# Kernel optimization log

Measured on AMD Instinct MI355X. Metric: run time of the kernel, lower is better.

## Reference

```python
import jax, jax.numpy as jnp
import numpy as np

B, H, W = 32, 64, 1024
D, L, HEADS, E, TOPK, HID, V = 256, 6, 8, 8, 2, 1024, 8000


def _conv(x, w, b, s):
    y = jax.lax.conv_general_dilated(x, w, (s, s), [(1, 1), (1, 1)],
                                     dimension_numbers=('NCHW', 'OIHW', 'NCHW'))
    return y + b[None, :, None, None]


def _gelu(v):
    return jax.nn.gelu(v, approximate=False)


def _ln(x, g, b):
    m = x.mean(-1, keepdims=True)
    v = jnp.mean((x - m) ** 2, -1, keepdims=True)
    return (x - m) * jax.lax.rsqrt(v + 1e-5) * g + b


def _pos(t, c):
    pos = jnp.arange(t, dtype=jnp.float32)[:, None]
    div = jnp.exp(jnp.arange(0, c, 2, dtype=jnp.float32) * (-np.log(10000.0) / c))
    pe = jnp.zeros((t, c), jnp.float32)
    pe = pe.at[:, 0::2].set(jnp.sin(pos * div)).at[:, 1::2].set(jnp.cos(pos * div))
    return pe[None]


def _mha(y, w, b, ow, ob):
    Bq, T, Dm = y.shape
    hd = Dm // HEADS
    qkv = y @ w.T + b
    q, k, v = jnp.split(qkv, 3, axis=-1)
    sh = lambda z: z.reshape(Bq, T, HEADS, hd).transpose(0, 2, 1, 3)
    q, k, v = sh(q), sh(k), sh(v)
    att = jax.nn.softmax(jnp.einsum('bhqd,bhkd->bhqk', q, k) / np.sqrt(hd).astype(np.float32), axis=-1)
    o = jnp.einsum('bhqk,bhkd->bhqd', att, v).transpose(0, 2, 1, 3).reshape(Bq, T, Dm)
    return o @ ow.T + ob


def _moe(y, rw, rb, w1, b1, w2, b2):
    logits = y @ rw.T + rb                      # [B,T,E]
    tlog, tidx = jax.lax.top_k(logits, TOPK)
    gates = jax.nn.softmax(tlog, axis=-1)        # [B,T,K]
    # combine weights per expert: sum_k gate_k * 1[idx_k == e]
    comb = jnp.sum(gates[..., None] * jax.nn.one_hot(tidx, E, dtype=y.dtype), axis=-2)  # [B,T,E]
    h = _gelu(jnp.einsum('btd,ehd->beth', y, w1) + b1[None, :, None, :])
    eo = jnp.einsum('beth,edh->betd', h, w2) + b2[None, :, None, :]
    out = jnp.einsum('bte,betd->btd', comb, eo)
    imp = jax.nn.softmax(logits, axis=-1).mean(axis=(0, 1))
    aux = jnp.mean((imp - 1.0 / E) ** 2)
    return out, aux


def _forward(x, cw1, cb1, cw2, cb2, cw3, cb3, cw4, cb4,
             ln1_g, ln1_b, qkv_w, qkv_b, out_w, out_b,
             ln2_g, ln2_b, router_w, router_b, e_w1, e_b1, e_w2, e_b2,
             normf_g, normf_b, head_w, head_b):
    f = _gelu(_conv(x, cw1, cb1, 2))
    f = _gelu(_conv(f, cw2, cb2, 2))
    f = _gelu(_conv(f, cw3, cb3, 2))
    f = _gelu(_conv(f, cw4, cb4, 1))          # [B,D,H/8,W/8]
    tok = f.mean(axis=2).transpose(0, 2, 1)    # [B,T,D], T=W/8
    h = tok + _pos(tok.shape[1], tok.shape[2])
    aux_total = jnp.asarray(0.0, h.dtype)
    for l in range(L):
        y = _mha(_ln(h, ln1_g[l], ln1_b[l]), qkv_w[l], qkv_b[l], out_w[l], out_b[l])
        h = h + y
        y, aux = _moe(_ln(h, ln2_g[l], ln2_b[l]), router_w[l], router_b[l],
                      e_w1[l], e_b1[l], e_w2[l], e_b2[l])
        h = h + y
        aux_total = aux_total + aux
    h = _ln(h, normf_g, normf_b)
    logits = h @ head_w.T + head_b
    return logits, aux_total / L


def setup_inputs() -> dict:
    key = jax.random.key(0)
    ks = iter(jax.random.split(key, 40))
    nrm = lambda shape: jax.random.normal(next(ks), shape, jnp.float32) * 0.02
    d = {}
    d['x'] = jax.random.normal(next(ks), (B, 1, H, W), jnp.float32)
    d['cw1'] = nrm((D // 4, 1, 3, 3));      d['cb1'] = jnp.zeros((D // 4,), jnp.float32)
    d['cw2'] = nrm((D // 2, D // 4, 3, 3)); d['cb2'] = jnp.zeros((D // 2,), jnp.float32)
    d['cw3'] = nrm((D, D // 2, 3, 3));      d['cb3'] = jnp.zeros((D,), jnp.float32)
    d['cw4'] = nrm((D, D, 3, 3));           d['cb4'] = jnp.zeros((D,), jnp.float32)
    d['ln1_g'] = jnp.ones((L, D), jnp.float32); d['ln1_b'] = jnp.zeros((L, D), jnp.float32)
    d['qkv_w'] = nrm((L, 3 * D, D));        d['qkv_b'] = jnp.zeros((L, 3 * D), jnp.float32)
    d['out_w'] = nrm((L, D, D));            d['out_b'] = jnp.zeros((L, D), jnp.float32)
    d['ln2_g'] = jnp.ones((L, D), jnp.float32); d['ln2_b'] = jnp.zeros((L, D), jnp.float32)
    d['router_w'] = nrm((L, E, D));         d['router_b'] = jnp.zeros((L, E), jnp.float32)
    d['e_w1'] = nrm((L, E, HID, D));        d['e_b1'] = jnp.zeros((L, E, HID), jnp.float32)
    d['e_w2'] = nrm((L, E, D, HID));        d['e_b2'] = jnp.zeros((L, E, D), jnp.float32)
    d['normf_g'] = jnp.ones((D,), jnp.float32); d['normf_b'] = jnp.zeros((D,), jnp.float32)
    d['head_w'] = nrm((V, D));              d['head_b'] = jnp.zeros((V,), jnp.float32)
    return d


def reference(x, cw1, cb1, cw2, cb2, cw3, cb3, cw4, cb4,
              ln1_g, ln1_b, qkv_w, qkv_b, out_w, out_b,
              ln2_g, ln2_b, router_w, router_b, e_w1, e_b1, e_w2, e_b2,
              normf_g, normf_b, head_w, head_b):
    return _forward(x, cw1, cb1, cw2, cb2, cw3, cb3, cw4, cb4,
                    ln1_g, ln1_b, qkv_w, qkv_b, out_w, out_b,
                    ln2_g, ln2_b, router_w, router_b, e_w1, e_b1, e_w2, e_b2,
                    normf_g, normf_b, head_w, head_b)
```

## Files before the change

### kernel.cpp

```cpp
#include <hip/hip_runtime.h>
#include <math.h>


__device__ __forceinline__ float gelu_f(float x) {
  return 0.5f * x * (1.0f + erff(x * 0.70710678118654752440f));
}

__global__ __launch_bounds__(256) void conv1_kernel(const float* __restrict__ x,
    const float* __restrict__ w, const float* __restrict__ bias, float* __restrict__ out) {
  int o = blockIdx.x * 256 + threadIdx.x;
  int co = o & 63, wo = (o >> 6) & 511, ho = (o >> 15) & 31, b = o >> 20;
  float acc = bias[co];
  const float* xp = x + (size_t)b * 65536;
  const float* wp = w + co * 9;
  #pragma unroll
  for (int kh = 0; kh < 3; kh++) {
    int hi = ho * 2 - 1 + kh;
    if ((unsigned)hi < 64u) {
      const float* row = xp + hi * 1024;
      #pragma unroll
      for (int kw = 0; kw < 3; kw++) {
        int wi = wo * 2 - 1 + kw;
        if ((unsigned)wi < 1024u) acc += row[wi] * wp[kh * 3 + kw];
      }
    }
  }
  out[o] = gelu_f(acc);
}

__global__ __launch_bounds__(256) void tr_cw_kernel(const float* __restrict__ w,
    float* __restrict__ o, int CI, int CO) {
  int i = blockIdx.x * 256 + threadIdx.x;
  if (i >= 9 * CI * CO) return;
  int co = i % CO; int r = i / CO; int ci = r % CI; int tap = r / CI;
  o[i] = w[(co * CI + ci) * 9 + tap];
}

template <int CI, int HI, int WI, int CO, int HO, int WO, int S>
__global__ __launch_bounds__(256) void convgemm8_kernel(
    const float* __restrict__ in, const float* __restrict__ wt,
    const float* __restrict__ bias, float* __restrict__ out) {
  __shared__ float As[16][132];
  __shared__ float Ws[16][132];
  int tid = threadIdx.x;
  int tileN = blockIdx.x * 128, tileM = blockIdx.y * 128;
  int tx = tid & 15, ty = tid >> 4;
  int ar = tid >> 1, ak = (tid & 1) << 3;
  int wk = tid >> 4, wc = (tid & 15) << 3;
  int m = tileM + ar;
  int wo = m % WO, ho = (m / WO) % HO, b = m / (WO * HO);
  float acc[8][8];
  #pragma unroll
  for (int i = 0; i < 8; i++)
    #pragma unroll
    for (int j = 0; j < 8; j++) acc[i][j] = 0.0f;
  for (int tap = 0; tap < 9; tap++) {
    int kh = tap / 3, kw = tap - kh * 3;
    int hi = ho * S - 1 + kh, wi = wo * S - 1 + kw;
    bool ok = ((unsigned)hi < (unsigned)HI) && ((unsigned)wi < (unsigned)WI);
    const float* ip = in + ((size_t)(b * HI + hi) * WI + wi) * CI + ak;
    const float* wp = wt + (size_t)tap * CI * CO + tileN + wc;
    for (int c0 = 0; c0 < CI; c0 += 16) {
      float4 a0 = {0.0f, 0.0f, 0.0f, 0.0f}, a1 = {0.0f, 0.0f, 0.0f, 0.0f};
      if (ok) {
        a0 = *(const float4*)(ip + c0);
        a1 = *(const float4*)(ip + c0 + 4);
      }
      float4 w0 = *(const float4*)(wp + (size_t)(c0 + wk) * CO);
      float4 w1 = *(const float4*)(wp + (size_t)(c0 + wk) * CO + 4);
      As[ak + 0][ar] = a0.x; As[ak + 1][ar] = a0.y; As[ak + 2][ar] = a0.z; As[ak + 3][ar] = a0.w;
      As[ak + 4][ar] = a1.x; As[ak + 5][ar] = a1.y; As[ak + 6][ar] = a1.z; As[ak + 7][ar] = a1.w;
      *(float4*)&Ws[wk][wc] = w0;
      *(float4*)&Ws[wk][wc + 4] = w1;
      __syncthreads();
      #pragma unroll
      for (int kk = 0; kk < 16; kk++) {
        float4 av0 = *(const float4*)&As[kk][ty << 2];
        float4 av1 = *(const float4*)&As[kk][(ty << 2) + 64];
        float4 wv0 = *(const float4*)&Ws[kk][tx << 2];
        float4 wv1 = *(const float4*)&Ws[kk][(tx << 2) + 64];
        float a[8] = {av0.x, av0.y, av0.z, av0.w, av1.x, av1.y, av1.z, av1.w};
        float w[8] = {wv0.x, wv0.y, wv0.z, wv0.w, wv1.x, wv1.y, wv1.z, wv1.w};
        #pragma unroll
        for (int i = 0; i < 8; i++)
          #pragma unroll
          for (int j = 0; j < 8; j++) acc[i][j] += a[i] * w[j];
      }
      __syncthreads();
    }
  }
  #pragma unroll
  for (int ih = 0; ih < 2; ih++) {
    #pragma unroll
    for (int i = 0; i < 4; i++) {
      float* Crow = out + (size_t)(tileM + ih * 64 + (ty << 2) + i) * CO + tileN;
      #pragma unroll
      for (int jh = 0; jh < 2; jh++) {
        #pragma unroll
        for (int j = 0; j < 4; j++) {
          int col = jh * 64 + (tx << 2) + j;
          Crow[col] = gelu_f(acc[ih * 4 + i][jh * 4 + j] + bias[tileN + col]);
        }
      }
    }
  }
}

__global__ __launch_bounds__(256) void gemm8_kernel(const float* __restrict__ A,
    const float* __restrict__ W, const float* __restrict__ bias, float* __restrict__ C,
    int N, int K, int addTo, int m0, int m1) {
  __shared__ float As[16][132];
  __shared__ float Ws[16][132];
  int tid = threadIdx.x;
  int tileN = blockIdx.x * 128, tileM = m0 + blockIdx.y * 128;
  int tx = tid & 15, ty = tid >> 4;
  int ar = tid >> 1, ak = (tid & 1) << 3;
  float acc[8][8];
  #pragma unroll
  for (int i = 0; i < 8; i++)
    #pragma unroll
    for (int j = 0; j < 8; j++) acc[i][j] = 0.0f;
  int arow = tileM + ar; if (arow > m1 - 1) arow = m1 - 1;
  int wrow = tileN + ar; if (wrow > N - 1) wrow = N - 1;
  const float* Ap = A + (size_t)arow * K + ak;
  const float* Wp = W + (size_t)wrow * K + ak;
  for (int k0 = 0; k0 < K; k0 += 16) {
    float4 a0 = *(const float4*)(Ap + k0);
    float4 a1 = *(const float4*)(Ap + k0 + 4);
    float4 w0 = *(const float4*)(Wp + k0);
    float4 w1 = *(const float4*)(Wp + k0 + 4);
    As[ak + 0][ar] = a0.x; As[ak + 1][ar] = a0.y; As[ak + 2][ar] = a0.z; As[ak + 3][ar] = a0.w;
    As[ak + 4][ar] = a1.x; As[ak + 5][ar] = a1.y; As[ak + 6][ar] = a1.z; As[ak + 7][ar] = a1.w;
    Ws[ak + 0][ar] = w0.x; Ws[ak + 1][ar] = w0.y; Ws[ak + 2][ar] = w0.z; Ws[ak + 3][ar] = w0.w;
    Ws[ak + 4][ar] = w1.x; Ws[ak + 5][ar] = w1.y; Ws[ak + 6][ar] = w1.z; Ws[ak + 7][ar] = w1.w;
    __syncthreads();
    #pragma unroll
    for (int kk = 0; kk < 16; kk++) {
      float4 av0 = *(const float4*)&As[kk][ty << 2];
      float4 av1 = *(const float4*)&As[kk][(ty << 2) + 64];
      float4 wv0 = *(const float4*)&Ws[kk][tx << 2];
      float4 wv1 = *(const float4*)&Ws[kk][(tx << 2) + 64];
      float a[8] = {av0.x, av0.y, av0.z, av0.w, av1.x, av1.y, av1.z, av1.w};
      float w[8] = {wv0.x, wv0.y, wv0.z, wv0.w, wv1.x, wv1.y, wv1.z, wv1.w};
      #pragma unroll
      for (int i = 0; i < 8; i++)
        #pragma unroll
        for (int j = 0; j < 8; j++) acc[i][j] += a[i] * w[j];
    }
    __syncthreads();
  }
  #pragma unroll
  for (int ih = 0; ih < 2; ih++) {
    #pragma unroll
    for (int i = 0; i < 4; i++) {
      int m = tileM + ih * 64 + (ty << 2) + i;
      if (m < m1) {
        float* Crow = C + (size_t)m * N;
        #pragma unroll
        for (int jh = 0; jh < 2; jh++) {
          #pragma unroll
          for (int j = 0; j < 4; j++) {
            int col = tileN + jh * 64 + (tx << 2) + j;
            if (col < N) {
              float v = acc[ih * 4 + i][jh * 4 + j] + bias[col];
              if (addTo) Crow[col] += v; else Crow[col] = v;
            }
          }
        }
      }
    }
  }
}

__global__ __launch_bounds__(256) void token_kernel(const float* __restrict__ f, float* __restrict__ h) {
  int i = blockIdx.x * 256 + threadIdx.x;
  int d = i & 255, t = (i >> 8) & 127, b = i >> 15;
  const float* fp = f + ((size_t)(b * 8) * 128 + t) * 256 + d;
  float s = 0.0f;
  #pragma unroll
  for (int ho = 0; ho < 8; ho++) s += fp[(size_t)ho * 32768];
  float tok = s * 0.125f;
  int i2 = d & ~1;
  float freq = expf(-(float)i2 * (float)(9.210340371976184 / 256.0));
  float ang = (float)t * freq;
  float pe = (d & 1) ? cosf(ang) : sinf(ang);
  h[i] = tok + pe;
}

__global__ __launch_bounds__(64) void ln_kernel(const float* __restrict__ in, float* __restrict__ out,
    const float* __restrict__ g, const float* __restrict__ b) {
  int row = blockIdx.x;
  int lane = threadIdx.x;
  float4 v = ((const float4*)(in + (size_t)row * 256))[lane];
  float s = v.x + v.y + v.z + v.w;
  float s2 = v.x * v.x + v.y * v.y + v.z * v.z + v.w * v.w;
  #pragma unroll
  for (int m = 1; m < 64; m <<= 1) { s += __shfl_xor(s, m); s2 += __shfl_xor(s2, m); }
  float mean = s * (1.0f / 256.0f);
  float var = s2 * (1.0f / 256.0f) - mean * mean;
  float rstd = rsqrtf(var + 1e-5f);
  float4 gv = ((const float4*)g)[lane];
  float4 bv = ((const float4*)b)[lane];
  float4 ov;
  ov.x = (v.x - mean) * rstd * gv.x + bv.x;
  ov.y = (v.y - mean) * rstd * gv.y + bv.y;
  ov.z = (v.z - mean) * rstd * gv.z + bv.z;
  ov.w = (v.w - mean) * rstd * gv.w + bv.w;
  ((float4*)(out + (size_t)row * 256))[lane] = ov;
}

__global__ __launch_bounds__(256) void gemm128_kernel(const float* __restrict__ A, const float* __restrict__ W,
    const float* __restrict__ bias, float* __restrict__ C, int N, int K, int addTo, int m0, int m1) {
  __shared__ float As[16][136];
  __shared__ float Ws[16][68];
  int tid = threadIdx.x;
  int tileN = blockIdx.x * 64, tileM = m0 + blockIdx.y * 128;
  int ar = tid >> 1, ak = (tid & 1) << 3;
  int wr = tid >> 2, wk = (tid & 3) << 2;
  int tx = tid & 15, ty = tid >> 4;
  float acc[8][4];
  #pragma unroll
  for (int i = 0; i < 8; i++)
    #pragma unroll
    for (int j = 0; j < 4; j++) acc[i][j] = 0.0f;
  int arow = tileM + ar; if (arow > m1 - 1) arow = m1 - 1;
  const float* Ap = A + (size_t)arow * K + ak;
  const float* Wp = W + (size_t)(tileN + wr) * K + wk;
  for (int k0 = 0; k0 < K; k0 += 16) {
    float4 a0 = *(const float4*)(Ap + k0);
    float4 a1 = *(const float4*)(Ap + k0 + 4);
    float4 w4 = *(const float4*)(Wp + k0);
    As[ak + 0][ar] = a0.x; As[ak + 1][ar] = a0.y; As[ak + 2][ar] = a0.z; As[ak + 3][ar] = a0.w;
    As[ak + 4][ar] = a1.x; As[ak + 5][ar] = a1.y; As[ak + 6][ar] = a1.z; As[ak + 7][ar] = a1.w;
    Ws[wk + 0][wr] = w4.x; Ws[wk + 1][wr] = w4.y; Ws[wk + 2][wr] = w4.z; Ws[wk + 3][wr] = w4.w;
    __syncthreads();
    #pragma unroll
    for (int kk = 0; kk < 16; kk++) {
      float4 av0 = *(const float4*)&As[kk][ty << 3];
      float4 av1 = *(const float4*)&As[kk][(ty << 3) + 4];
      float4 wv = *(const float4*)&Ws[kk][tx << 2];
      float a[8] = {av0.x, av0.y, av0.z, av0.w, av1.x, av1.y, av1.z, av1.w};
      float w[4] = {wv.x, wv.y, wv.z, wv.w};
      #pragma unroll
      for (int i = 0; i < 8; i++)
        #pragma unroll
        for (int j = 0; j < 4; j++) acc[i][j] += a[i] * w[j];
    }
    __syncthreads();
  }
  #pragma unroll
  for (int i = 0; i < 8; i++) {
    int m = tileM + (ty << 3) + i;
    if (m < m1) {
      float* Crow = C + (size_t)m * N + tileN + (tx << 2);
      #pragma unroll
      for (int j = 0; j < 4; j++) {
        float v = acc[i][j] + bias[tileN + (tx << 2) + j];
        if (addTo) Crow[j] += v; else Crow[j] = v;
      }
    }
  }
}

__global__ __launch_bounds__(256) void gemm_kernel(const float* __restrict__ A, const float* __restrict__ W,
    const float* __restrict__ bias, float* __restrict__ C, int N, int K, int addTo, int m0, int m1) {
  __shared__ float As[16][68];
  __shared__ float Ws[16][68];
  int tid = threadIdx.x;
  int tileN = blockIdx.x * 64, tileM = m0 + blockIdx.y * 64;
  int lr = tid >> 2, lk = (tid & 3) << 2;
  int tx = tid & 15, ty = tid >> 4;
  float acc[4][4];
  #pragma unroll
  for (int i = 0; i < 4; i++)
    #pragma unroll
    for (int j = 0; j < 4; j++) acc[i][j] = 0.0f;
  int arow = tileM + lr; if (arow > m1 - 1) arow = m1 - 1;
  const float* Ap = A + (size_t)arow * K + lk;
  const float* Wp = W + (size_t)(tileN + lr) * K + lk;
  for (int k0 = 0; k0 < K; k0 += 16) {
    float4 a4 = *(const float4*)(Ap + k0);
    float4 w4 = *(const float4*)(Wp + k0);
    As[lk + 0][lr] = a4.x; As[lk + 1][lr] = a4.y; As[lk + 2][lr] = a4.z; As[lk + 3][lr] = a4.w;
    Ws[lk + 0][lr] = w4.x; Ws[lk + 1][lr] = w4.y; Ws[lk + 2][lr] = w4.z; Ws[lk + 3][lr] = w4.w;
    __syncthreads();
    #pragma unroll
    for (int kk = 0; kk < 16; kk++) {
      float4 av = *(const float4*)&As[kk][ty << 2];
      float4 wv = *(const float4*)&Ws[kk][tx << 2];
      float a[4] = {av.x, av.y, av.z, av.w};
      float w[4] = {wv.x, wv.y, wv.z, wv.w};
      #pragma unroll
      for (int i = 0; i < 4; i++)
        #pragma unroll
        for (int j = 0; j < 4; j++) acc[i][j] += a[i] * w[j];
    }
    __syncthreads();
  }
  #pragma unroll
  for (int i = 0; i < 4; i++) {
    int m = tileM + (ty << 2) + i;
    if (m < m1) {
      float* Crow = C + (size_t)m * N + tileN + (tx << 2);
      #pragma unroll
      for (int j = 0; j < 4; j++) {
        float v = acc[i][j] + bias[tileN + (tx << 2) + j];
        if (addTo) Crow[j] += v; else Crow[j] = v;
      }
    }
  }
}

__global__ __launch_bounds__(256) void head_row0_kernel(const float* __restrict__ y,
    const float* __restrict__ W, const float* __restrict__ bias, float* __restrict__ out) {
  __shared__ float yrow[256];
  int tid = threadIdx.x;
  yrow[tid] = y[tid];
  __syncthreads();
  for (int col = tid; col < 8000; col += 256) {
    const float4* wp = (const float4*)(W + (size_t)col * 256);
    float acc = 0.0f;
    for (int d = 0; d < 64; d++) {
      float4 w4 = wp[d];
      acc += w4.x * yrow[d * 4] + w4.y * yrow[d * 4 + 1] + w4.z * yrow[d * 4 + 2] + w4.w * yrow[d * 4 + 3];
    }
    out[col] = acc + bias[col];
  }
}

__global__ __launch_bounds__(128) void attn_kernel(const float* __restrict__ qkv, float* __restrict__ o) {
  __shared__ float Ks[128][33];
  __shared__ float Vs[128][33];
  int b = blockIdx.x >> 3, hh = blockIdx.x & 7;
  int t = threadIdx.x;
  const float* base = qkv + (size_t)(b * 128 + t) * 768 + hh * 32;
  float q[32];
  #pragma unroll
  for (int i = 0; i < 32; i += 4) {
    float4 v4 = *(const float4*)(base + i);
    q[i] = v4.x; q[i + 1] = v4.y; q[i + 2] = v4.z; q[i + 3] = v4.w;
    float4 k4 = *(const float4*)(base + 256 + i);
    Ks[t][i] = k4.x; Ks[t][i + 1] = k4.y; Ks[t][i + 2] = k4.z; Ks[t][i + 3] = k4.w;
    float4 w4 = *(const float4*)(base + 512 + i);
    Vs[t][i] = w4.x; Vs[t][i + 1] = w4.y; Vs[t][i + 2] = w4.z; Vs[t][i + 3] = w4.w;
  }
  __syncthreads();
  const float scale = 0.17677669529663687f;
  float m = -1e30f;
  for (int j = 0; j < 128; j++) {
    float s = 0.0f;
    #pragma unroll
    for (int i = 0; i < 32; i++) s += q[i] * Ks[j][i];
    m = fmaxf(m, s);
  }
  m *= scale;
  float l = 0.0f;
  float acc[32];
  #pragma unroll
  for (int i = 0; i < 32; i++) acc[i] = 0.0f;
  for (int j = 0; j < 128; j++) {
    float s = 0.0f;
    #pragma unroll
    for (int i = 0; i < 32; i++) s += q[i] * Ks[j][i];
    float p = __expf(s * scale - m);
    l += p;
    #pragma unroll
    for (int i = 0; i < 32; i++) acc[i] += p * Vs[j][i];
  }
  float inv = 1.0f / l;
  float* op = o + (size_t)(b * 128 + t) * 256 + hh * 32;
  #pragma unroll
  for (int i = 0; i < 32; i++) op[i] = acc[i] * inv;
}

__global__ __launch_bounds__(256) void router_kernel(const float* __restrict__ y,
    const float* __restrict__ rw, const float* __restrict__ rb,
    int* __restrict__ eidx, float* __restrict__ egate, float* __restrict__ imp) {
  int token = blockIdx.x * 256 + threadIdx.x;
  const float4* yp4 = (const float4*)(y + (size_t)token * 256);
  float logit[8];
  #pragma unroll
  for (int e = 0; e < 8; e++) {
    const float4* wp = (const float4*)(rw + e * 256);
    float acc = 0.0f;
    for (int d = 0; d < 64; d++) {
      float4 w4 = wp[d]; float4 v4 = yp4[d];
      acc += w4.x * v4.x + w4.y * v4.y + w4.z * v4.z + w4.w * v4.w;
    }
    logit[e] = acc + rb[e];
  }
  float mx = logit[0];
  #pragma unroll
  for (int e = 1; e < 8; e++) mx = fmaxf(mx, logit[e]);
  float p[8]; float sum = 0.0f;
  #pragma unroll
  for (int e = 0; e < 8; e++) { p[e] = __expf(logit[e] - mx); sum += p[e]; }
  float inv = 1.0f / sum;
  #pragma unroll
  for (int e = 0; e < 8; e++) {
    float pe = p[e] * inv;
    #pragma unroll
    for (int msk = 1; msk < 64; msk <<= 1) pe += __shfl_xor(pe, msk);
    if ((threadIdx.x & 63) == 0) atomicAdd(&imp[e], pe);
  }
  float m0 = -1e30f, m1 = -1e30f; int i0 = 0, i1 = 0;
  #pragma unroll
  for (int e = 0; e < 8; e++) {
    if (logit[e] > m0) { m1 = m0; i1 = i0; m0 = logit[e]; i0 = e; }
    else if (logit[e] > m1) { m1 = logit[e]; i1 = e; }
  }
  float g1 = __expf(m1 - m0);
  float g0 = 1.0f / (1.0f + g1);
  g1 *= g0;
  eidx[token * 2] = i0; eidx[token * 2 + 1] = i1;
  egate[token * 2] = g0; egate[token * 2 + 1] = g1;
}

__global__ __launch_bounds__(256) void tr_w1_kernel(const float* __restrict__ w, float4* __restrict__ o) {
  int i = blockIdx.x * 256 + threadIdx.x;
  int r = i & 1023, d4 = (i >> 10) & 63, e = i >> 16;
  o[i] = *(const float4*)(w + ((size_t)(e * 1024 + r)) * 256 + (d4 << 2));
}
__global__ __launch_bounds__(256) void tr_w2_kernel(const float* __restrict__ w, float4* __restrict__ o) {
  int i = blockIdx.x * 256 + threadIdx.x;
  int dd = i & 255, j4 = (i >> 8) & 255, e = i >> 16;
  o[i] = *(const float4*)(w + ((size_t)(e * 256 + dd)) * 1024 + (j4 << 2));
}

__global__ __launch_bounds__(256) void moe_kernel(const float* __restrict__ y,
    const float4* __restrict__ w1t, const float* __restrict__ b1,
    const float4* __restrict__ w2t, const float* __restrict__ b2,
    const int* __restrict__ eidx, const float* __restrict__ egate,
    float* __restrict__ h) {
  __shared__ float4 ylds[16][64];
  __shared__ __align__(16) float hlds[16][512];
  __shared__ int list[128];
  __shared__ int cnt;
  int tid = threadIdx.x;
  int e = blockIdx.x >> 7;
  int c = (blockIdx.x >> 1) & 63;
  int jc = blockIdx.x & 1;
  if (tid == 0) cnt = 0;
  __syncthreads();
  if (tid < 128) {
    int s = c * 128 + tid;
    if (eidx[s] == e) list[atomicAdd(&cnt, 1)] = s;
  }
  __syncthreads();
  int n = cnt;
  if (n == 0) return;
  int g8 = tid >> 7;
  int dd = tid & 127;
  const float4* w1p = w1t + (size_t)e * 65536 + jc * 512 + tid;
  const float4* w2p = w2t + (size_t)e * 65536 + dd;
  float bb0 = b1[e * 1024 + jc * 512 + tid];
  float bb1 = b1[e * 1024 + jc * 512 + 256 + tid];
  float b2v0 = jc ? 0.0f : b2[e * 256 + dd];
  float b2v1 = jc ? 0.0f : b2[e * 256 + dd + 128];
  const float4* y4 = (const float4*)y;
  for (int base = 0; base < n; base += 16) {
    int nt = (n - base) < 16 ? (n - base) : 16;
    for (int idx = tid; idx < 16 * 64; idx += 256) {
      int ti = idx >> 6, d4 = idx & 63;
      int slot = list[base + (ti < nt ? ti : 0)];
      ylds[ti][d4] = y4[(size_t)(slot >> 1) * 64 + d4];
    }
    __syncthreads();
    float h0[16], h1[16];
    #pragma unroll
    for (int i = 0; i < 16; i++) { h0[i] = bb0; h1[i] = bb1; }
    for (int d4 = 0; d4 < 64; d4++) {
      float4 wa = w1p[(size_t)d4 * 1024];
      float4 wb = w1p[(size_t)d4 * 1024 + 256];
      #pragma unroll
      for (int i = 0; i < 16; i++) {
        float4 yv = ylds[i][d4];
        h0[i] += wa.x * yv.x + wa.y * yv.y + wa.z * yv.z + wa.w * yv.w;
        h1[i] += wb.x * yv.x + wb.y * yv.y + wb.z * yv.z + wb.w * yv.w;
      }
    }
    #pragma unroll
    for (int i = 0; i < 16; i++) {
      hlds[i][tid] = gelu_f(h0[i]);
      hlds[i][256 + tid] = gelu_f(h1[i]);
    }
    __syncthreads();
    float acc2a[8], acc2b[8];
    #pragma unroll
    for (int i = 0; i < 8; i++) { acc2a[i] = 0.0f; acc2b[i] = 0.0f; }
    for (int j4 = 0; j4 < 128; j4++) {
      float4 wa = w2p[(size_t)(jc * 128 + j4) * 256];
      float4 wb = w2p[(size_t)(jc * 128 + j4) * 256 + 128];
      #pragma unroll
      for (int i = 0; i < 8; i++) {
        float4 hv = *(const float4*)&hlds[g8 * 8 + i][j4 * 4];
        acc2a[i] += wa.x * hv.x + wa.y * hv.y + wa.z * hv.z + wa.w * hv.w;
        acc2b[i] += wb.x * hv.x + wb.y * hv.y + wb.z * hv.z + wb.w * hv.w;
      }
    }
    __syncthreads();
    #pragma unroll
    for (int i = 0; i < 8; i++) {
      int ii = g8 * 8 + i;
      if (ii < nt) {
        int slot = list[base + ii];
        float g = egate[slot];
        float* hp = h + (size_t)(slot >> 1) * 256;
        atomicAdd(hp + dd, g * (acc2a[i] + b2v0));
        atomicAdd(hp + dd + 128, g * (acc2b[i] + b2v1));
      }
    }
  }
}

__global__ void zero_kernel(float* __restrict__ p, int n) {
  int i = blockIdx.x * blockDim.x + threadIdx.x;
  if (i < n) p[i] = 0.0f;
}

__global__ void aux_kernel(const float* __restrict__ imp, float* __restrict__ out) {
  float total = 0.0f;
  for (int l = 0; l < 6; l++) {
    float a = 0.0f;
    for (int e = 0; e < 8; e++) {
      float v = imp[l * 8 + e] * (1.0f / 4096.0f) - 0.125f;
      a += v * v;
    }
    total += a * 0.125f;
  }
  out[0] = total * (1.0f / 6.0f);
}

extern "C" void kernel_launch(void* const* d_in, const int* in_sizes, int n_in,
                              void* d_out, int out_size, void* d_ws, size_t ws_size,
                              hipStream_t stream) {
  const float* x      = (const float*)d_in[0];
  const float* cw1    = (const float*)d_in[1];
  const float* cb1    = (const float*)d_in[2];
  const float* cw2    = (const float*)d_in[3];
  const float* cb2    = (const float*)d_in[4];
  const float* cw3    = (const float*)d_in[5];
  const float* cb3    = (const float*)d_in[6];
  const float* cw4    = (const float*)d_in[7];
  const float* cb4    = (const float*)d_in[8];
  const float* ln1_g  = (const float*)d_in[9];
  const float* ln1_b  = (const float*)d_in[10];
  const float* qkv_w  = (const float*)d_in[11];
  const float* qkv_b  = (const float*)d_in[12];
  const float* out_w  = (const float*)d_in[13];
  const float* out_b  = (const float*)d_in[14];
  const float* ln2_g  = (const float*)d_in[15];
  const float* ln2_b  = (const float*)d_in[16];
  const float* router_w = (const float*)d_in[17];
  const float* router_b = (const float*)d_in[18];
  const float* e_w1   = (const float*)d_in[19];
  const float* e_b1   = (const float*)d_in[20];
  const float* e_w2   = (const float*)d_in[21];
  const float* e_b2   = (const float*)d_in[22];
  const float* normf_g = (const float*)d_in[23];
  const float* normf_b = (const float*)d_in[24];
  const float* head_w = (const float*)d_in[25];
  const float* head_b = (const float*)d_in[26];
  float* out = (float*)d_out;
  (void)d_ws; (void)ws_size;

  float* y = out;
  float* h = out + 1048576;
  float* S = out + 2097152;
  float* c2 = S;
  float* c1 = S + 16777216;
  float* c3 = S + 16777216;
  float* c4 = S;
  float* cw2t = S + 25165824;
  float* cw3t = S + 25239552;
  float* cw4t = S + 25534464;
  float* qkvb = S;
  float* ob   = S + 3145728;
  float* y2   = S + 4194304;
  int*   eidx  = (int*)(S + 5242880);
  float* egate = S + 5242880 + 8192;
  float* imp   = S + 5242880 + 16384;
  float* w1t   = S + 5767168;
  float* w2t   = S + 7864320;

  tr_cw_kernel<<<(9 * 64 * 128 + 255) / 256, 256, 0, stream>>>(cw2, cw2t, 64, 128);
  tr_cw_kernel<<<(9 * 128 * 256 + 255) / 256, 256, 0, stream>>>(cw3, cw3t, 128, 256);
  tr_cw_kernel<<<(9 * 256 * 256 + 255) / 256, 256, 0, stream>>>(cw4, cw4t, 256, 256);

  for (int c = 0; c < 4; c++) {
    const float* xc = x + (size_t)c * 8 * 65536;
    conv1_kernel<<<32768, 256, 0, stream>>>(xc, cw1, cb1, c1);
    convgemm8_kernel<64, 32, 512, 128, 16, 256, 2>
        <<<dim3(1, 256), 256, 0, stream>>>(c1, cw2t, cb2, c2 + (size_t)c * 4194304);
  }
  convgemm8_kernel<128, 16, 256, 256, 8, 128, 2>
      <<<dim3(2, 256), 256, 0, stream>>>(c2, cw3t, cb3, c3);
  convgemm8_kernel<256, 8, 128, 256, 8, 128, 1>
      <<<dim3(2, 256), 256, 0, stream>>>(c3, cw4t, cb4, c4);
  token_kernel<<<4096, 256, 0, stream>>>(c4, h);
  zero_kernel<<<1, 64, 0, stream>>>(imp, 48);

  for (int l = 0; l < 6; l++) {
    tr_w1_kernel<<<2048, 256, 0, stream>>>(e_w1 + (size_t)l * 8 * 1024 * 256, (float4*)w1t);
    tr_w2_kernel<<<2048, 256, 0, stream>>>(e_w2 + (size_t)l * 8 * 256 * 1024, (float4*)w2t);
    ln_kernel<<<4096, 64, 0, stream>>>(h, y, ln1_g + l * 256, ln1_b + l * 256);
    gemm128_kernel<<<dim3(12, 32), 256, 0, stream>>>(y, qkv_w + (size_t)l * 768 * 256, qkv_b + l * 768,
                                                     qkvb, 768, 256, 0, 0, 4096);
    attn_kernel<<<256, 128, 0, stream>>>(qkvb, ob);
    gemm128_kernel<<<dim3(4, 32), 256, 0, stream>>>(ob, out_w + (size_t)l * 256 * 256, out_b + l * 256,
                                                    h, 256, 256, 1, 0, 4096);
    ln_kernel<<<4096, 64, 0, stream>>>(h, y2, ln2_g + l * 256, ln2_b + l * 256);
    router_kernel<<<16, 256, 0, stream>>>(y2, router_w + l * 8 * 256, router_b + l * 8,
                                          eidx, egate, imp + l * 8);
    moe_kernel<<<1024, 256, 0, stream>>>(y2, (const float4*)w1t, e_b1 + l * 8 * 1024,
                                         (const float4*)w2t, e_b2 + l * 8 * 256,
                                         eidx, egate, h);
  }

  ln_kernel<<<4096, 64, 0, stream>>>(h, y, normf_g, normf_b);
  aux_kernel<<<1, 1, 0, stream>>>(imp, out + 32768000);

  gemm8_kernel<<<dim3(63, 31), 256, 0, stream>>>(y, head_w, head_b, out, 8000, 256, 0, 132, 4096);
  gemm8_kernel<<<dim3(63, 1), 256, 0, stream>>>(y, head_w, head_b, out, 8000, 256, 0, 5, 132);
  gemm_kernel<<<dim3(125, 1), 256, 0, stream>>>(y, head_w, head_b, out, 8000, 256, 0, 1, 5);
  head_row0_kernel<<<1, 256, 0, stream>>>(y, head_w, head_b, out);
}
```

Before: 5.434 ms.

## Run conv layers 2-4 on bf16 MFMA with split hi/lo precision

Replaces the FP32 SIMT implicit-GEMM convolution kernel with one built on MFMA 16x16x32 bf16 instructions. Each FP32 operand is split into bf16 high and low parts, and three MFMAs per tile (hi*hi, lo*hi, hi*lo) approximate FP32 accuracy. The weight transpose now writes bf16 hi/lo arrays in a K-contiguous layout, and activations are split into hi/lo on the fly while being staged into shared memory. This trades three matrix-core passes plus conversion work against the much lower throughput of scalar FP32 FMAs, with a small loss of precision.

```diff
diff --git a/kernel.cpp b/kernel.cpp
--- a/kernel.cpp
+++ b/kernel.cpp
@@ -1,6 +1,9 @@
 #include <hip/hip_runtime.h>
 #include <math.h>
 
+
+typedef __bf16 bf16x8 __attribute__((ext_vector_type(8)));
+typedef float f32x4 __attribute__((ext_vector_type(4)));
 
 __device__ __forceinline__ float gelu_f(float x) {
   return 0.5f * x * (1.0f + erff(x * 0.70710678118654752440f));
@@ -28,80 +31,103 @@
   out[o] = gelu_f(acc);
 }
 
-__global__ __launch_bounds__(256) void tr_cw_kernel(const float* __restrict__ w,
-    float* __restrict__ o, int CI, int CO) {
+__global__ __launch_bounds__(256) void tr_cw_bf16_kernel(const float* __restrict__ w,
+    __bf16* __restrict__ hi, __bf16* __restrict__ lo, int CI, int CO) {
   int i = blockIdx.x * 256 + threadIdx.x;
   if (i >= 9 * CI * CO) return;
-  int co = i % CO; int r = i / CO; int ci = r % CI; int tap = r / CI;
-  o[i] = w[(co * CI + ci) * 9 + tap];
+  int ci = i % CI; int r = i / CI; int co = r % CO; int tap = r / CO;
+  float x = w[(co * CI + ci) * 9 + tap];
+  __bf16 h = (__bf16)x;
+  __bf16 l = (__bf16)(x - (float)h);
+  hi[i] = h; lo[i] = l;
 }
 
 template <int CI, int HI, int WI, int CO, int HO, int WO, int S>
-__global__ __launch_bounds__(256) void convgemm8_kernel(
-    const float* __restrict__ in, const float* __restrict__ wt,
-    const float* __restrict__ bias, float* __restrict__ out) {
-  __shared__ float As[16][132];
-  __shared__ float Ws[16][132];
+__global__ __launch_bounds__(256) void convmfma_kernel(
+    const float* __restrict__ in, const __bf16* __restrict__ wthi,
+    const __bf16* __restrict__ wtlo, const float* __restrict__ bias,
+    float* __restrict__ out) {
+  __shared__ __bf16 Ah[128 * 40], Al[128 * 40], Bh[128 * 40], Bl[128 * 40];
   int tid = threadIdx.x;
+  int lane = tid & 63, wid = tid >> 6;
+  int wr = (wid >> 1) << 6, wc = (wid & 1) << 6;
+  int lr = lane & 15;
+  int lk = (lane >> 4) << 3;
   int tileN = blockIdx.x * 128, tileM = blockIdx.y * 128;
-  int tx = tid & 15, ty = tid >> 4;
-  int ar = tid >> 1, ak = (tid & 1) << 3;
-  int wk = tid >> 4, wc = (tid & 15) << 3;
-  int m = tileM + ar;
+  int tr = tid >> 1;
+  int tk = (tid & 1) << 4;
+  int m = tileM + tr;
   int wo = m % WO, ho = (m / WO) % HO, b = m / (WO * HO);
-  float acc[8][8];
-  #pragma unroll
-  for (int i = 0; i < 8; i++)
-    #pragma unroll
-    for (int j = 0; j < 8; j++) acc[i][j] = 0.0f;
+  f32x4 acc[4][4];
+  #pragma unroll
+  for (int i = 0; i < 4; i++)
+    #pragma unroll
+    for (int j = 0; j < 4; j++) acc[i][j] = (f32x4){0.f, 0.f, 0.f, 0.f};
+
   for (int tap = 0; tap < 9; tap++) {
     int kh = tap / 3, kw = tap - kh * 3;
-    int hi = ho * S - 1 + kh, wi = wo * S - 1 + kw;
-    bool ok = ((unsigned)hi < (unsigned)HI) && ((unsigned)wi < (unsigned)WI);
-    const float* ip = in + ((size_t)(b * HI + hi) * WI + wi) * CI + ak;
-    const float* wp = wt + (size_t)tap * CI * CO + tileN + wc;
-    for (int c0 = 0; c0 < CI; c0 += 16) {
-      float4 a0 = {0.0f, 0.0f, 0.0f, 0.0f}, a1 = {0.0f, 0.0f, 0.0f, 0.0f};
-      if (ok) {
-        a0 = *(const float4*)(ip + c0);
-        a1 = *(const float4*)(ip + c0 + 4);
-      }
-      float4 w0 = *(const float4*)(wp + (size_t)(c0 + wk) * CO);
-      float4 w1 = *(const float4*)(wp + (size_t)(c0 + wk) * CO + 4);
-      As[ak + 0][ar] = a0.x; As[ak + 1][ar] = a0.y; As[ak + 2][ar] = a0.z; As[ak + 3][ar] = a0.w;
-      As[ak + 4][ar] = a1.x; As[ak + 5][ar] = a1.y; As[ak + 6][ar] = a1.z; As[ak + 7][ar] = a1.w;
-      *(float4*)&Ws[wk][wc] = w0;
-      *(float4*)&Ws[wk][wc + 4] = w1;
+    int hi_ = ho * S - 1 + kh, wi_ = wo * S - 1 + kw;
+    bool ok = ((unsigned)hi_ < (unsigned)HI) && ((unsigned)wi_ < (unsigned)WI);
+    const float* ip = in + ((size_t)(b * HI + hi_) * WI + wi_) * CI + tk;
+    const __bf16* wph = wthi + ((size_t)tap * CO + tileN + tr) * CI + tk;
+    const __bf16* wpl = wtlo + ((size_t)tap * CO + tileN + tr) * CI + tk;
+    for (int c0 = 0; c0 < CI; c0 += 32) {
+      float v[16];
+      #pragma unroll
+      for (int q = 0; q < 4; q++) {
+        float4 t4 = ok ? *(const float4*)(ip + c0 + q * 4) : (float4){0.f, 0.f, 0.f, 0.f};
+        v[q * 4 + 0] = t4.x; v[q * 4 + 1] = t4.y; v[q * 4 + 2] = t4.z; v[q * 4 + 3] = t4.w;
+      }
+      bf16x8 hv0, hv1, lv0, lv1;
+      #pragma unroll
+      for (int j = 0; j < 8; j++) {
+        __bf16 h0 = (__bf16)v[j];       hv0[j] = h0;
+        lv0[j] = (__bf16)(v[j] - (float)h0);
+        __bf16 h1 = (__bf16)v[8 + j];   hv1[j] = h1;
+        lv1[j] = (__bf16)(v[8 + j] - (float)h1);
+      }
+      *(bf16x8*)&Ah[tr * 40 + tk] = hv0;
+      *(bf16x8*)&Ah[tr * 40 + tk + 8] = hv1;
+      *(bf16x8*)&Al[tr * 40 + tk] = lv0;
+      *(bf16x8*)&Al[tr * 40 + tk + 8] = lv1;
+      *(uint4*)&Bh[tr * 40 + tk] = *(const uint4*)(wph + c0);
+      *(uint4*)&Bh[tr * 40 + tk + 8] = *(const uint4*)(wph + c0 + 8);
+      *(uint4*)&Bl[tr * 40 + tk] = *(const uint4*)(wpl + c0);
+      *(uint4*)&Bl[tr * 40 + tk + 8] = *(const uint4*)(wpl + c0 + 8);
       __syncthreads();
-      #pragma unroll
-      for (int kk = 0; kk < 16; kk++) {
-        float4 av0 = *(const float4*)&As[kk][ty << 2];
-        float4 av1 = *(const float4*)&As[kk][(ty << 2) + 64];
-        float4 wv0 = *(const float4*)&Ws[kk][tx << 2];
-        float4 wv1 = *(const float4*)&Ws[kk][(tx << 2) + 64];
-        float a[8] = {av0.x, av0.y, av0.z, av0.w, av1.x, av1.y, av1.z, av1.w};
-        float w[8] = {wv0.x, wv0.y, wv0.z, wv0.w, wv1.x, wv1.y, wv1.z, wv1.w};
+      bf16x8 ah[4], al[4];
+      #pragma unroll
+      for (int mt = 0; mt < 4; mt++) {
+        int r = wr + mt * 16 + lr;
+        ah[mt] = *(const bf16x8*)&Ah[r * 40 + lk];
+        al[mt] = *(const bf16x8*)&Al[r * 40 + lk];
+      }
+      #pragma unroll
+      for (int nt = 0; nt < 4; nt++) {
+        int cc = wc + nt * 16 + lr;
+        bf16x8 bh = *(const bf16x8*)&Bh[cc * 40 + lk];
+        bf16x8 bl = *(const bf16x8*)&Bl[cc * 40 + lk];
         #pragma unroll
-        for (int i = 0; i < 8; i++)
-          #pragma unroll
-          for (int j = 0; j < 8; j++) acc[i][j] += a[i] * w[j];
+        for (int mt = 0; mt < 4; mt++) {
+          acc[mt][nt] = __builtin_amdgcn_mfma_f32_16x16x32_bf16(ah[mt], bh, acc[mt][nt], 0, 0, 0);
+          acc[mt][nt] = __builtin_amdgcn_mfma_f32_16x16x32_bf16(al[mt], bh, acc[mt][nt], 0, 0, 0);
+          acc[mt][nt] = __builtin_amdgcn_mfma_f32_16x16x32_bf16(ah[mt], bl, acc[mt][nt], 0, 0, 0);
+        }
       }
       __syncthreads();
     }
   }
-  #pragma unroll
-  for (int ih = 0; ih < 2; ih++) {
-    #pragma unroll
-    for (int i = 0; i < 4; i++) {
-      float* Crow = out + (size_t)(tileM + ih * 64 + (ty << 2) + i) * CO + tileN;
-      #pragma unroll
-      for (int jh = 0; jh < 2; jh++) {
-        #pragma unroll
-        for (int j = 0; j < 4; j++) {
-          int col = jh * 64 + (tx << 2) + j;
-          Crow[col] = gelu_f(acc[ih * 4 + i][jh * 4 + j] + bias[tileN + col]);
-        }
-      }
+  int drow = (lane >> 4) << 2;
+  #pragma unroll
+  for (int mt = 0; mt < 4; mt++) {
+    #pragma unroll
+    for (int nt = 0; nt < 4; nt++) {
+      int orow = tileM + wr + mt * 16 + drow;
+      int ocol = tileN + wc + nt * 16 + lr;
+      float bv = bias[ocol];
+      #pragma unroll
+      for (int r = 0; r < 4; r++)
+        out[(size_t)(orow + r) * CO + ocol] = gelu_f(acc[mt][nt][r] + bv);
     }
   }
 }
@@ -571,9 +597,12 @@
   float* c1 = S + 16777216;
   float* c3 = S + 16777216;
   float* c4 = S;
-  float* cw2t = S + 25165824;
-  float* cw3t = S + 25239552;
-  float* cw4t = S + 25534464;
+  __bf16* cw2h = (__bf16*)(S + 25165824);
+  __bf16* cw2l = (__bf16*)(S + 25202688);
+  __bf16* cw3h = (__bf16*)(S + 25239552);
+  __bf16* cw3l = (__bf16*)(S + 25387008);
+  __bf16* cw4h = (__bf16*)(S + 25534464);
+  __bf16* cw4l = (__bf16*)(S + 25829376);
   float* qkvb = S;
   float* ob   = S + 3145728;
   float* y2   = S + 4194304;
@@ -583,20 +612,20 @@
   float* w1t   = S + 5767168;
   float* w2t   = S + 7864320;
 
-  tr_cw_kernel<<<(9 * 64 * 128 + 255) / 256, 256, 0, stream>>>(cw2, cw2t, 64, 128);
-  tr_cw_kernel<<<(9 * 128 * 256 + 255) / 256, 256, 0, stream>>>(cw3, cw3t, 128, 256);
-  tr_cw_kernel<<<(9 * 256 * 256 + 255) / 256, 256, 0, stream>>>(cw4, cw4t, 256, 256);
+  tr_cw_bf16_kernel<<<(9 * 64 * 128 + 255) / 256, 256, 0, stream>>>(cw2, cw2h, cw2l, 64, 128);
+  tr_cw_bf16_kernel<<<(9 * 128 * 256 + 255) / 256, 256, 0, stream>>>(cw3, cw3h, cw3l, 128, 256);
+  tr_cw_bf16_kernel<<<(9 * 256 * 256 + 255) / 256, 256, 0, stream>>>(cw4, cw4h, cw4l, 256, 256);
 
   for (int c = 0; c < 4; c++) {
     const float* xc = x + (size_t)c * 8 * 65536;
     conv1_kernel<<<32768, 256, 0, stream>>>(xc, cw1, cb1, c1);
-    convgemm8_kernel<64, 32, 512, 128, 16, 256, 2>
-        <<<dim3(1, 256), 256, 0, stream>>>(c1, cw2t, cb2, c2 + (size_t)c * 4194304);
-  }
-  convgemm8_kernel<128, 16, 256, 256, 8, 128, 2>
-      <<<dim3(2, 256), 256, 0, stream>>>(c2, cw3t, cb3, c3);
-  convgemm8_kernel<256, 8, 128, 256, 8, 128, 1>
-      <<<dim3(2, 256), 256, 0, stream>>>(c3, cw4t, cb4, c4);
+    convmfma_kernel<64, 32, 512, 128, 16, 256, 2>
+        <<<dim3(1, 256), 256, 0, stream>>>(c1, cw2h, cw2l, cb2, c2 + (size_t)c * 4194304);
+  }
+  convmfma_kernel<128, 16, 256, 256, 8, 128, 2>
+      <<<dim3(2, 256), 256, 0, stream>>>(c2, cw3h, cw3l, cb3, c3);
+  convmfma_kernel<256, 8, 128, 256, 8, 128, 1>
+      <<<dim3(2, 256), 256, 0, stream>>>(c3, cw4h, cw4l, cb4, c4);
   token_kernel<<<4096, 256, 0, stream>>>(c4, h);
   zero_kernel<<<1, 64, 0, stream>>>(imp, 48);
 
```

Result: faster. 4.589 ms (-15.5%).
